# Kernel tuning notes

Measured on AMD Instinct MI355X. Metric: run time of the kernel, lower is better.

The kernel has to match this reference:

```python
import jax, jax.numpy as jnp
import numpy as np

B, L, D, H, HID = 2048, 512, 17, 8, 256  # batch, max entities, feat dim, heads, mlp hidden
SPECIAL, OUT = 9, 23  # special vector dims, policy logits (7+16)


def _lin(k, out_d, in_d, scale):
    kw, kb = jax.random.split(k)
    W = jax.random.normal(kw, (out_d, in_d), jnp.float32) * scale
    b = jax.random.normal(kb, (out_d,), jnp.float32) * 0.01
    return W, b


def setup_inputs() -> dict:
    key = jax.random.key(0)
    ks = jax.random.split(key, 16)
    # observations: row 0 holds the 9-dim special vector, rows 1..L are ragged entities
    x = jax.random.normal(ks[0], (B, L + 1, D), jnp.float32)
    lengths = jax.random.randint(ks[1], (B,), 1, L + 1)
    mask = (jnp.arange(L)[None, :] < lengths[:, None]).astype(jnp.float32)
    x = x.at[:, 1:, :].multiply(mask[:, :, None])  # zero rows mark padding
    s = 1.0 / np.sqrt(D)
    # per-head K/V projections (num_heads separate tiny Linears)
    Wk = jax.random.normal(ks[2], (H, D, D), jnp.float32) * s
    bk = jax.random.normal(ks[3], (H, D), jnp.float32) * 0.01
    Wv = jax.random.normal(ks[4], (H, D, D), jnp.float32) * s
    bv = jax.random.normal(ks[5], (H, D), jnp.float32) * 0.01
    q = jax.random.normal(ks[6], (H, D), jnp.float32)  # learned per-head queries
    Wo, bo = _lin(ks[7], D, H * D, 1.0 / np.sqrt(H * D))
    sc = 1.0 / np.sqrt(D + SPECIAL)
    pW1, pb1 = _lin(ks[8], HID, D + SPECIAL, sc)
    pW2, pb2 = _lin(ks[9], HID, HID, 1.0 / np.sqrt(HID))
    pW3, pb3 = _lin(ks[10], OUT, HID, 1.0 / np.sqrt(HID))
    vW1, vb1 = _lin(ks[11], HID, D + SPECIAL, sc)
    vW2, vb2 = _lin(ks[12], HID, HID, 1.0 / np.sqrt(HID))
    vW3, vb3 = _lin(ks[13], 1, HID, 1.0 / np.sqrt(HID))
    return dict(x=x, Wk=Wk, bk=bk, Wv=Wv, bv=bv, q=q, Wo=Wo, bo=bo,
                pW1=pW1, pb1=pb1, pW2=pW2, pb2=pb2, pW3=pW3, pb3=pb3,
                vW1=vW1, vb1=vb1, vW2=vW2, vb2=vb2, vW3=vW3, vb3=vb3)


def _mlp(h, W1, b1, W2, b2, W3, b3):
    h = jax.nn.relu(h @ W1.T + b1)
    h = jax.nn.relu(h @ W2.T + b2)
    return h @ W3.T + b3


def reference(x, Wk, bk, Wv, bv, q, Wo, bo,
              pW1, pb1, pW2, pb2, pW3, pb3,
              vW1, vb1, vW2, vb2, vW3, vb3):
    special = x[:, 0, :SPECIAL]            # [B, 9]
    seq = x[:, 1:, :]                      # [B, L, D]
    mask = jnp.sum(jnp.abs(seq), axis=-1) != 0  # [B, L] non-padded rows
    # per-head keys/values for all samples at once (batched over the head loop)
    keys = jnp.einsum('bld,hed->bhle', seq, Wk) + bk[None, :, None, :]   # [B,H,L,D]
    vals = jnp.einsum('bld,hed->bhle', seq, Wv) + bv[None, :, None, :]   # [B,H,L,D]
    scores = jnp.einsum('bhle,he->bhl', keys, q)                          # [B,H,L]
    scores = jnp.where(mask[:, None, :], scores, -1e9)
    w = jax.nn.softmax(scores, axis=-1)                                   # [B,H,L]
    agg = jnp.einsum('bhl,bhle->bhe', w, vals).reshape(x.shape[0], H * D)  # concat heads
    attn = agg @ Wo.T + bo                                                # [B, D]
    comb = jnp.concatenate([attn, special], axis=-1)                      # [B, D+9]
    logits = _mlp(comb, pW1, pb1, pW2, pb2, pW3, pb3)                     # [B, 23]
    value = _mlp(comb, vW1, vb1, vW2, vb2, vW3, vb3)                      # [B, 1]
    return logits, value
```

## Files before the change

### kernel.cpp

```cpp
#include <hip/hip_runtime.h>
#include <hip/hip_bf16.h>

#define B_ 2048
#define D_ 17
#define H_ 8
#define HID_ 256
#define OUT_ 23
#define XROW 8721
#define SEQN 8704

__device__ __forceinline__ float4 ld4u(const float* p) {
  float4 v; __builtin_memcpy(&v, p, 16); return v;
}
__device__ __forceinline__ float bclane(float v, int l) {
  return __uint_as_float(__builtin_amdgcn_readlane(__float_as_uint(v), l));
}

__global__ __launch_bounds__(256) void prep_kernel(
    const float* __restrict__ pW2, const float* __restrict__ vW2,
    const float* __restrict__ Wk, const float* __restrict__ bk,
    const float* __restrict__ q,
    float* __restrict__ pW2t, float* __restrict__ vW2t, float* __restrict__ qkc)
{
  const int bid = blockIdx.x;
  const int t = threadIdx.x;
  if (bid == 128) {
    if (t < H_ * D_) {
      const int h = t / D_, dd = t - h * D_;
      float s = 0.f;
      #pragma unroll
      for (int e = 0; e < D_; ++e) s = fmaf(Wk[h*289 + e*D_ + dd], q[h*D_ + e], s);
      qkc[h*18 + dd] = s;
    } else if (t < H_ * D_ + H_) {
      const int h = t - H_ * D_;
      float s = 0.f;
      #pragma unroll
      for (int e = 0; e < D_; ++e) s = fmaf(bk[h*D_ + e], q[h*D_ + e], s);
      qkc[h*18 + 17] = s;
    }
    return;
  }
  __shared__ float tile[32][33];
  const int m = bid >> 6, tid = bid & 63;
  const int ti = (tid >> 3) * 32, tk = (tid & 7) * 32;
  const float* src = m ? vW2 : pW2;
  float* dst = m ? vW2t : pW2t;
  const int tx = t & 31, ty = t >> 5;
  #pragma unroll
  for (int r = 0; r < 4; ++r) tile[ty + 8*r][tx] = src[(ti + ty + 8*r)*HID_ + tk + tx];
  __syncthreads();
  #pragma unroll
  for (int r = 0; r < 4; ++r) dst[(tk + ty + 8*r)*HID_ + ti + tx] = tile[tx][ty + 8*r];
}

__global__ __launch_bounds__(256, 3) void attn_comb_kernel(
    const float* __restrict__ x, const float* __restrict__ qkc,
    const float* __restrict__ Wv, const float* __restrict__ bv,
    const float* __restrict__ Wo, const float* __restrict__ bo,
    float* __restrict__ comb)
{
  __shared__ __align__(16) float s_seq[SEQN];
  __shared__ float s_part[4][H_][18];
  __shared__ float s_swn[136];
  __shared__ float s_agg[136];
  __shared__ float s_wp[136];

  const int t = threadIdx.x;
  const int b = blockIdx.x;
  const int w = t >> 6, lane = t & 63;
  const int hp = lane >> 4;
  const int rg = lane & 15;
  const float* xb = x + (size_t)b * XROW;
  const float* xs = xb + D_;

  const float pv = xs[(size_t)lane * 136];
  const unsigned long long live = __ballot(pv != 0.f) | 1ull;
  const int nrows = 8 * (64 - __builtin_clzll(live));

  {
    const int rounds = (nrows * D_ + 1023) >> 10;
    float4 st[9];
    #pragma unroll
    for (int j = 0; j < 9; ++j) if (j < rounds) {
      int off = ((j << 8) + t) << 2; if (off > SEQN - 4) off = SEQN - 4;
      st[j] = ld4u(xs + off);
    }
    #pragma unroll
    for (int j = 0; j < 9; ++j) if (j < rounds) {
      int off = ((j << 8) + t) << 2; if (off > SEQN - 4) off = SEQN - 4;
      *(float4*)&s_seq[off] = st[j];
    }
  }

  const float* q0 = qkc + (2*hp) * 18;
  float qk0[D_], qk1[D_];
  #pragma unroll
  for (int d = 0; d < D_; ++d) { qk0[d] = q0[d]; qk1[d] = q0[18 + d]; }
  const float ch0 = q0[17], ch1 = q0[35];

  __syncthreads();

  const int ng = nrows >> 2;
  float den0 = 0.f, den1 = 0.f;
  float acc0[D_], acc1[D_];
  #pragma unroll
  for (int d = 0; d < D_; ++d) { acc0[d] = 0.f; acc1[d] = 0.f; }

  auto dorow = [&](const float* f, bool ok) {
    float s0 = ch0, s1 = ch1;
    #pragma unroll
    for (int d = 0; d < D_; ++d) { s0 = fmaf(qk0[d], f[d], s0); s1 = fmaf(qk1[d], f[d], s1); }
    const bool lv = ok && (f[0] != 0.f);
    const float p0 = lv ? __expf(s0) : 0.f;
    const float p1 = lv ? __expf(s1) : 0.f;
    den0 += p0; den1 += p1;
    #pragma unroll
    for (int d = 0; d < D_; ++d) {
      acc0[d] = fmaf(p0, f[d], acc0[d]);
      acc1[d] = fmaf(p1, f[d], acc1[d]);
    }
  };
  auto dogran = [&](int g, bool ok) {
    const float* gb = &s_seq[(ok ? g : 0) * 68];
    {
      float f[36];
      #pragma unroll
      for (int i = 0; i < 9; ++i) {
        const float4 v = *(const float4*)(gb + 4*i);
        f[4*i] = v.x; f[4*i+1] = v.y; f[4*i+2] = v.z; f[4*i+3] = v.w;
      }
      dorow(&f[0], ok); dorow(&f[17], ok);
    }
    {
      float f[36];
      #pragma unroll
      for (int i = 0; i < 9; ++i) {
        const float4 v = *(const float4*)(gb + 32 + 4*i);
        f[4*i] = v.x; f[4*i+1] = v.y; f[4*i+2] = v.z; f[4*i+3] = v.w;
      }
      dorow(&f[2], ok); dorow(&f[19], ok);
    }
  };

  {
    const int g = w * 16 + rg;
    dogran(g, g < ng);
  }
  if (ng > 64) {
    const int g = w * 16 + rg + 64;
    dogran(g, g < ng);
  }

  #pragma unroll
  for (int m = 1; m <= 8; m <<= 1) {
    den0 += __shfl_xor(den0, m, 64);
    den1 += __shfl_xor(den1, m, 64);
    #pragma unroll
    for (int d = 0; d < D_; ++d) {
      acc0[d] += __shfl_xor(acc0[d], m, 64);
      acc1[d] += __shfl_xor(acc1[d], m, 64);
    }
  }
  if (rg == 0) {
    float* p0p = &s_part[w][2*hp][0];
    float* p1p = &s_part[w][2*hp + 1][0];
    p0p[0] = den0; p1p[0] = den1;
    #pragma unroll
    for (int d = 0; d < D_; ++d) { p0p[1 + d] = acc0[d]; p1p[1 + d] = acc1[d]; }
  }
  __syncthreads();

  if (t < 136) {
    const int hh = t / D_, d = t - hh * D_;
    float dn = 0.f, ac = 0.f;
    #pragma unroll
    for (int ww = 0; ww < 4; ++ww) { dn += s_part[ww][hh][0]; ac += s_part[ww][hh][1 + d]; }
    s_swn[t] = ac / dn;
  }
  __syncthreads();
  if (t < 136) {
    const int hh = t / D_, e = t - hh * D_;
    float s = bv[t];
    #pragma unroll
    for (int d = 0; d < D_; ++d) s = fmaf(Wv[hh*289 + e*D_ + d], s_swn[hh*D_ + d], s);
    s_agg[t] = s;
  }
  __syncthreads();
  if (t < 136) {
    const int o = t >> 3, pt = t & 7;
    float s = 0.f;
    #pragma unroll
    for (int j = 0; j < D_; ++j) s = fmaf(Wo[o*136 + pt*D_ + j], s_agg[pt*D_ + j], s);
    s_wp[t] = s;
  }
  __syncthreads();
  if (t < D_) {
    float s = bo[t];
    #pragma unroll
    for (int pt = 0; pt < 8; ++pt) s += s_wp[t*8 + pt];
    comb[b*26 + t] = s;
  } else if (t < 26) {
    comb[b*26 + t] = xb[t - D_];
  }
}

__global__ __launch_bounds__(512) void mlp_kernel(
    const float* __restrict__ comb,
    const float* __restrict__ pW1, const float* __restrict__ pb1,
    const float* __restrict__ pW2t, const float* __restrict__ pb2,
    const float* __restrict__ pW3, const float* __restrict__ pb3,
    const float* __restrict__ vW1, const float* __restrict__ vb1,
    const float* __restrict__ vW2t, const float* __restrict__ vb2,
    const float* __restrict__ vW3, const float* __restrict__ vb3,
    float* __restrict__ out)
{
  __shared__ float s_comb[8][26];
  __shared__ __align__(16) float s_red[2][3][8][HID_];
  __shared__ __align__(16) float s_h2[2][8][HID_];

  const int t = threadIdx.x;
  const int b0 = blockIdx.x * 8;
  const int p = t >> 8;
  const int kq = (t >> 6) & 3;
  const int ln = t & 63;

  if (t < 208) { const int bb = t / 26, k = t - bb*26; s_comb[bb][k] = comb[(size_t)(b0 + bb)*26 + k]; }
  __syncthreads();

  const float* W1  = p ? vW1  : pW1;   const float* B1 = p ? vb1 : pb1;
  const float* W2t = p ? vW2t : pW2t;  const float* B2 = p ? vb2 : pb2;

  float h[8];
  {
    const int i = kq * 64 + ln;
    float a[8];
    #pragma unroll
    for (int bb = 0; bb < 8; ++bb) a[bb] = 0.f;
    const float* wr = W1 + i * 26;
    for (int k = 0; k < 26; ++k) {
      const float wk = wr[k];
      #pragma unroll
      for (int bb = 0; bb < 8; ++bb) a[bb] = fmaf(wk, s_comb[bb][k], a[bb]);
    }
    const float bias = B1[i];
    #pragma unroll
    for (int bb = 0; bb < 8; ++bb) h[bb] = fmaxf(a[bb] + bias, 0.f);
  }

  float4 acc[8];
  #pragma unroll
  for (int bb = 0; bb < 8; ++bb) acc[bb] = make_float4(0.f, 0.f, 0.f, 0.f);
  {
    const float* wbase = W2t + (size_t)(kq * 64) * HID_ + 4 * ln;
    #pragma unroll 8
    for (int jj = 0; jj < 64; ++jj) {
      const float4 wv = *(const float4*)(wbase + (size_t)jj * HID_);
      #pragma unroll
      for (int bb = 0; bb < 8; ++bb) {
        const float hv = bclane(h[bb], jj);
        acc[bb].x = fmaf(wv.x, hv, acc[bb].x);
        acc[bb].y = fmaf(wv.y, hv, acc[bb].y);
        acc[bb].z = fmaf(wv.z, hv, acc[bb].z);
        acc[bb].w = fmaf(wv.w, hv, acc[bb].w);
      }
    }
  }
  if (kq > 0) {
    #pragma unroll
    for (int bb = 0; bb < 8; ++bb) *(float4*)&s_red[p][kq - 1][bb][4 * ln] = acc[bb];
  }
  __syncthreads();
  if (kq == 0) {
    const float4 bias = *(const float4*)&B2[4 * ln];
    #pragma unroll
    for (int bb = 0; bb < 8; ++bb) {
      const float4 r0 = *(const float4*)&s_red[p][0][bb][4 * ln];
      const float4 r1 = *(const float4*)&s_red[p][1][bb][4 * ln];
      const float4 r2 = *(const float4*)&s_red[p][2][bb][4 * ln];
      float4 rr;
      rr.x = fmaxf(acc[bb].x + r0.x + r1.x + r2.x + bias.x, 0.f);
      rr.y = fmaxf(acc[bb].y + r0.y + r1.y + r2.y + bias.y, 0.f);
      rr.z = fmaxf(acc[bb].z + r0.z + r1.z + r2.z + bias.z, 0.f);
      rr.w = fmaxf(acc[bb].w + r0.w + r1.w + r2.w + bias.w, 0.f);
      *(float4*)&s_h2[p][bb][4 * ln] = rr;
    }
  }
  __syncthreads();

  if (t < 184) {
    const int bb = t / OUT_, o = t - bb * OUT_;
    const float4* w4 = (const float4*)(pW3 + o * HID_);
    const float4* h4 = (const float4*)&s_h2[0][bb][0];
    float s = pb3[o];
    for (int k = 0; k < 64; ++k) {
      const float4 wv = w4[k], hv = h4[k];
      s = fmaf(wv.x, hv.x, fmaf(wv.y, hv.y, fmaf(wv.z, hv.z, fmaf(wv.w, hv.w, s))));
    }
    out[(size_t)(b0 + bb) * OUT_ + o] = s;
  } else if (t >= 256 && t < 264) {
    const int bb = t - 256;
    const float4* w4 = (const float4*)vW3;
    const float4* h4 = (const float4*)&s_h2[1][bb][0];
    float s = vb3[0];
    for (int k = 0; k < 64; ++k) {
      const float4 wv = w4[k], hv = h4[k];
      s = fmaf(wv.x, hv.x, fmaf(wv.y, hv.y, fmaf(wv.z, hv.z, fmaf(wv.w, hv.w, s))));
    }
    out[(size_t)B_ * OUT_ + b0 + bb] = s;
  }
}

extern "C" void kernel_launch(void* const* d_in, const int* in_sizes, int n_in,
                              void* d_out, int out_size, void* d_ws, size_t ws_size,
                              hipStream_t stream) {
  (void)in_sizes; (void)n_in; (void)out_size; (void)ws_size;
  const float* x   = (const float*)d_in[0];
  const float* Wk  = (const float*)d_in[1];
  const float* bk  = (const float*)d_in[2];
  const float* Wv  = (const float*)d_in[3];
  const float* bv  = (const float*)d_in[4];
  const float* q   = (const float*)d_in[5];
  const float* Wo  = (const float*)d_in[6];
  const float* bo  = (const float*)d_in[7];
  const float* pW1 = (const float*)d_in[8];
  const float* pb1 = (const float*)d_in[9];
  const float* pW2 = (const float*)d_in[10];
  const float* pb2 = (const float*)d_in[11];
  const float* pW3 = (const float*)d_in[12];
  const float* pb3 = (const float*)d_in[13];
  const float* vW1 = (const float*)d_in[14];
  const float* vb1 = (const float*)d_in[15];
  const float* vW2 = (const float*)d_in[16];
  const float* vb2 = (const float*)d_in[17];
  const float* vW3 = (const float*)d_in[18];
  const float* vb3 = (const float*)d_in[19];
  float* out = (float*)d_out;

  float* pW2t = (float*)d_ws;
  float* vW2t = pW2t + (size_t)HID_ * HID_;
  float* qkc  = vW2t + (size_t)HID_ * HID_;
  float* comb = qkc + 160;

  prep_kernel<<<129, 256, 0, stream>>>(pW2, vW2, Wk, bk, q, pW2t, vW2t, qkc);
  attn_comb_kernel<<<B_, 256, 0, stream>>>(x, qkc, Wv, bv, Wo, bo, comb);
  mlp_kernel<<<B_ / 8, 512, 0, stream>>>(comb, pW1, pb1, pW2t, pb2, pW3, pb3,
                                         vW1, vb1, vW2t, vb2, vW3, vb3, out);
}
```

Measured before the change: 54.61 us.

## Pad staged sequence rows to stride 20 in LDS for aligned per-row loads

```diff
diff --git a/kernel.cpp b/kernel.cpp
--- a/kernel.cpp
+++ b/kernel.cpp
@@ -8,6 +8,7 @@
 #define OUT_ 23
 #define XROW 8721
 #define SEQN 8704
+#define ROWP 20
 
 __device__ __forceinline__ float4 ld4u(const float* p) {
   float4 v; __builtin_memcpy(&v, p, 16); return v;
@@ -53,13 +54,25 @@
   for (int r = 0; r < 4; ++r) dst[(tk + ty + 8*r)*HID_ + ti + tx] = tile[tx][ty + 8*r];
 }
 
+__device__ __forceinline__ void stage_write(float* s_seq, int off, float4 v) {
+  const int r = off / 17;
+  const int c = off - r * 17;
+  int c1 = c + 1, r1 = r; if (c1 >= 17) { c1 -= 17; ++r1; }
+  int c2 = c + 2, r2 = r; if (c2 >= 17) { c2 -= 17; ++r2; }
+  int c3 = c + 3, r3 = r; if (c3 >= 17) { c3 -= 17; ++r3; }
+  s_seq[r  * ROWP + c ] = v.x;
+  s_seq[r1 * ROWP + c1] = v.y;
+  s_seq[r2 * ROWP + c2] = v.z;
+  s_seq[r3 * ROWP + c3] = v.w;
+}
+
 __global__ __launch_bounds__(256, 3) void attn_comb_kernel(
     const float* __restrict__ x, const float* __restrict__ qkc,
     const float* __restrict__ Wv, const float* __restrict__ bv,
     const float* __restrict__ Wo, const float* __restrict__ bo,
     float* __restrict__ comb)
 {
-  __shared__ __align__(16) float s_seq[SEQN];
+  __shared__ __align__(16) float s_seq[512 * ROWP];
   __shared__ float s_part[4][H_][18];
   __shared__ float s_swn[136];
   __shared__ float s_agg[136];
@@ -76,20 +89,29 @@
   const float pv = xs[(size_t)lane * 136];
   const unsigned long long live = __ballot(pv != 0.f) | 1ull;
   const int nrows = 8 * (64 - __builtin_clzll(live));
+  const int rounds = (nrows * D_ + 1023) >> 10;
 
   {
-    const int rounds = (nrows * D_ + 1023) >> 10;
-    float4 st[9];
-    #pragma unroll
-    for (int j = 0; j < 9; ++j) if (j < rounds) {
-      int off = ((j << 8) + t) << 2; if (off > SEQN - 4) off = SEQN - 4;
-      st[j] = ld4u(xs + off);
-    }
-    #pragma unroll
-    for (int j = 0; j < 9; ++j) if (j < rounds) {
-      int off = ((j << 8) + t) << 2; if (off > SEQN - 4) off = SEQN - 4;
-      *(float4*)&s_seq[off] = st[j];
-    }
+    const int base = t * 4;
+    float4 s0, s1, s2, s3, s4, s5, s6, s7, s8;
+    s0 = ld4u(xs + base);
+    if (rounds > 1) s1 = ld4u(xs + base + 1024);
+    if (rounds > 2) s2 = ld4u(xs + base + 2048);
+    if (rounds > 3) s3 = ld4u(xs + base + 3072);
+    if (rounds > 4) s4 = ld4u(xs + base + 4096);
+    if (rounds > 5) s5 = ld4u(xs + base + 5120);
+    if (rounds > 6) s6 = ld4u(xs + base + 6144);
+    if (rounds > 7) s7 = ld4u(xs + base + 7168);
+    if (rounds > 8) { int o8 = base + 8192; if (o8 > SEQN - 4) o8 = SEQN - 4; s8 = ld4u(xs + o8); }
+    stage_write(s_seq, base, s0);
+    if (rounds > 1) stage_write(s_seq, base + 1024, s1);
+    if (rounds > 2) stage_write(s_seq, base + 2048, s2);
+    if (rounds > 3) stage_write(s_seq, base + 3072, s3);
+    if (rounds > 4) stage_write(s_seq, base + 4096, s4);
+    if (rounds > 5) stage_write(s_seq, base + 5120, s5);
+    if (rounds > 6) stage_write(s_seq, base + 6144, s6);
+    if (rounds > 7) stage_write(s_seq, base + 7168, s7);
+    if (rounds > 8) { int o8 = base + 8192; if (o8 > SEQN - 4) o8 = SEQN - 4; stage_write(s_seq, o8, s8); }
   }
 
   const float* q0 = qkc + (2*hp) * 18;
@@ -100,55 +122,75 @@
 
   __syncthreads();
 
-  const int ng = nrows >> 2;
   float den0 = 0.f, den1 = 0.f;
   float acc0[D_], acc1[D_];
   #pragma unroll
   for (int d = 0; d < D_; ++d) { acc0[d] = 0.f; acc1[d] = 0.f; }
 
-  auto dorow = [&](const float* f, bool ok) {
-    float s0 = ch0, s1 = ch1;
-    #pragma unroll
-    for (int d = 0; d < D_; ++d) { s0 = fmaf(qk0[d], f[d], s0); s1 = fmaf(qk1[d], f[d], s1); }
-    const bool lv = ok && (f[0] != 0.f);
-    const float p0 = lv ? __expf(s0) : 0.f;
-    const float p1 = lv ? __expf(s1) : 0.f;
+  auto dorow = [&](int row) {
+    const bool ok = row < nrows;
+    const float* rp = &s_seq[(ok ? row : 0) * ROWP];
+    const float4 v0 = *(const float4*)rp;
+    const float4 v1 = *(const float4*)(rp + 4);
+    const float4 v2 = *(const float4*)(rp + 8);
+    const float4 v3 = *(const float4*)(rp + 12);
+    const float4 v4 = *(const float4*)(rp + 16);
+    float sA = ch0, sB = ch1;
+    sA = fmaf(qk0[0],  v0.x, sA); sB = fmaf(qk1[0],  v0.x, sB);
+    sA = fmaf(qk0[1],  v0.y, sA); sB = fmaf(qk1[1],  v0.y, sB);
+    sA = fmaf(qk0[2],  v0.z, sA); sB = fmaf(qk1[2],  v0.z, sB);
+    sA = fmaf(qk0[3],  v0.w, sA); sB = fmaf(qk1[3],  v0.w, sB);
+    sA = fmaf(qk0[4],  v1.x, sA); sB = fmaf(qk1[4],  v1.x, sB);
+    sA = fmaf(qk0[5],  v1.y, sA); sB = fmaf(qk1[5],  v1.y, sB);
+    sA = fmaf(qk0[6],  v1.z, sA); sB = fmaf(qk1[6],  v1.z, sB);
+    sA = fmaf(qk0[7],  v1.w, sA); sB = fmaf(qk1[7],  v1.w, sB);
+    sA = fmaf(qk0[8],  v2.x, sA); sB = fmaf(qk1[8],  v2.x, sB);
+    sA = fmaf(qk0[9],  v2.y, sA); sB = fmaf(qk1[9],  v2.y, sB);
+    sA = fmaf(qk0[10], v2.z, sA); sB = fmaf(qk1[10], v2.z, sB);
+    sA = fmaf(qk0[11], v2.w, sA); sB = fmaf(qk1[11], v2.w, sB);
+    sA = fmaf(qk0[12], v3.x, sA); sB = fmaf(qk1[12], v3.x, sB);
+    sA = fmaf(qk0[13], v3.y, sA); sB = fmaf(qk1[13], v3.y, sB);
+    sA = fmaf(qk0[14], v3.z, sA); sB = fmaf(qk1[14], v3.z, sB);
+    sA = fmaf(qk0[15], v3.w, sA); sB = fmaf(qk1[15], v3.w, sB);
+    sA = fmaf(qk0[16], v4.x, sA); sB = fmaf(qk1[16], v4.x, sB);
+    const bool lv = ok && (v0.x != 0.f);
+    const float p0 = lv ? __expf(sA) : 0.f;
+    const float p1 = lv ? __expf(sB) : 0.f;
     den0 += p0; den1 += p1;
-    #pragma unroll
-    for (int d = 0; d < D_; ++d) {
-      acc0[d] = fmaf(p0, f[d], acc0[d]);
-      acc1[d] = fmaf(p1, f[d], acc1[d]);
-    }
+    acc0[0]  = fmaf(p0, v0.x, acc0[0]);  acc1[0]  = fmaf(p1, v0.x, acc1[0]);
+    acc0[1]  = fmaf(p0, v0.y, acc0[1]);  acc1[1]  = fmaf(p1, v0.y, acc1[1]);
+    acc0[2]  = fmaf(p0, v0.z, acc0[2]);  acc1[2]  = fmaf(p1, v0.z, acc1[2]);
+    acc0[3]  = fmaf(p0, v0.w, acc0[3]);  acc1[3]  = fmaf(p1, v0.w, acc1[3]);
+    acc0[4]  = fmaf(p0, v1.x, acc0[4]);  acc1[4]  = fmaf(p1, v1.x, acc1[4]);
+    acc0[5]  = fmaf(p0, v1.y, acc0[5]);  acc1[5]  = fmaf(p1, v1.y, acc1[5]);
+    acc0[6]  = fmaf(p0, v1.z, acc0[6]);  acc1[6]  = fmaf(p1, v1.z, acc1[6]);
+    acc0[7]  = fmaf(p0, v1.w, acc0[7]);  acc1[7]  = fmaf(p1, v1.w, acc1[7]);
+    acc0[8]  = fmaf(p0, v2.x, acc0[8]);  acc1[8]  = fmaf(p1, v2.x, acc1[8]);
+    acc0[9]  = fmaf(p0, v2.y, acc0[9]);  acc1[9]  = fmaf(p1, v2.y, acc1[9]);
+    acc0[10] = fmaf(p0, v2.z, acc0[10]); acc1[10] = fmaf(p1, v2.z, acc1[10]);
+    acc0[11] = fmaf(p0, v2.w, acc0[11]); acc1[11] = fmaf(p1, v2.w, acc1[11]);
+    acc0[12] = fmaf(p0, v3.x, acc0[12]); acc1[12] = fmaf(p1, v3.x, acc1[12]);
+    acc0[13] = fmaf(p0, v3.y, acc0[13]); acc1[13] = fmaf(p1, v3.y, acc1[13]);
+    acc0[14] = fmaf(p0, v3.z, acc0[14]); acc1[14] = fmaf(p1, v3.z, acc1[14]);
+    acc0[15] = fmaf(p0, v3.w, acc0[15]); acc1[15] = fmaf(p1, v3.w, acc1[15]);
+    acc0[16] = fmaf(p0, v4.x, acc0[16]); acc1[16] = fmaf(p1, v4.x, acc1[16]);
   };
-  auto dogran = [&](int g, bool ok) {
-    const float* gb = &s_seq[(ok ? g : 0) * 68];
-    {
-      float f[36];
-      #pragma unroll
-      for (int i = 0; i < 9; ++i) {
-        const float4 v = *(const float4*)(gb + 4*i);
-        f[4*i] = v.x; f[4*i+1] = v.y; f[4*i+2] = v.z; f[4*i+3] = v.w;
-      }
-      dorow(&f[0], ok); dorow(&f[17], ok);
-    }
-    {
-      float f[36];
-      #pragma unroll
-      for (int i = 0; i < 9; ++i) {
-        const float4 v = *(const float4*)(gb + 32 + 4*i);
-        f[4*i] = v.x; f[4*i+1] = v.y; f[4*i+2] = v.z; f[4*i+3] = v.w;
-      }
-      dorow(&f[2], ok); dorow(&f[19], ok);
-    }
-  };
 
   {
-    const int g = w * 16 + rg;
-    dogran(g, g < ng);
-  }
-  if (ng > 64) {
-    const int g = w * 16 + rg + 64;
-    dogran(g, g < ng);
+    const int s0r = w * 64;
+    if (s0r < nrows) {
+      dorow(s0r + rg);
+      dorow(s0r + rg + 16);
+      dorow(s0r + rg + 32);
+      dorow(s0r + rg + 48);
+    }
+    const int s1r = 256 + w * 64;
+    if (s1r < nrows) {
+      dorow(s1r + rg);
+      dorow(s1r + rg + 16);
+      dorow(s1r + rg + 32);
+      dorow(s1r + rg + 48);
+    }
   }
 
   #pragma unroll
```

Measured after the change: 56.16 us. 2.8% more time.
